# Kernel tuning notes

Measured on AMD Instinct MI355X. Metric: run time of the kernel, lower is better.

The kernel has to match this reference:

```python
import jax, jax.numpy as jnp
import numpy as np

L, D, H, FF = 4, 256, 8, 1024
B, S = 4, 1024
HD = D // H
EPS = 1e-5


def layer_norm(x, g, b):
    mu = jnp.mean(x, axis=-1, keepdims=True)
    var = jnp.mean(jnp.square(x - mu), axis=-1, keepdims=True)
    return (x - mu) * jax.lax.rsqrt(var + EPS) * g + b


def setup_inputs() -> dict:
    key = jax.random.key(0)
    ks = jax.random.split(key, 16)
    sd = 0.02
    return {
        "x": jax.random.normal(ks[0], (B, S, D), dtype=jnp.float32),
        "mask": jnp.ones((B, S), dtype=jnp.int32),
        # per-layer stacked params (leading dim L); Linear stored as (in, out)
        "qkv_w": jax.random.normal(ks[1], (L, D, 3 * D), dtype=jnp.float32) * sd,
        "qkv_b": jnp.zeros((L, 3 * D), dtype=jnp.float32),
        "fc_w": jax.random.normal(ks[2], (L, D, D), dtype=jnp.float32) * sd,
        "fc_b": jnp.zeros((L, D), dtype=jnp.float32),
        "ln1_g": jnp.ones((L, D), dtype=jnp.float32),
        "ln1_b": jnp.zeros((L, D), dtype=jnp.float32),
        "ln2_g": jnp.ones((L, D), dtype=jnp.float32),
        "ln2_b": jnp.zeros((L, D), dtype=jnp.float32),
        "ff1_w": jax.random.normal(ks[3], (L, D, FF), dtype=jnp.float32) * sd,
        "ff1_b": jnp.zeros((L, FF), dtype=jnp.float32),
        "ff2_w": jax.random.normal(ks[4], (L, FF, D), dtype=jnp.float32) * sd,
        "ff2_b": jnp.zeros((L, D), dtype=jnp.float32),
    }


def reference(x, mask, qkv_w, qkv_b, fc_w, fc_b, ln1_g, ln1_b, ln2_g, ln2_b,
              ff1_w, ff1_b, ff2_w, ff2_b):
    # mask: 1 = valid token, 0 = pad
    neg_inf = jnp.finfo(x.dtype).min
    key_mask = (mask == 0)[:, None, None, :]  # [B,1,1,S]
    for l in range(L):
        residual = x
        qkv = x @ qkv_w[l] + qkv_b[l]                       # [B,S,3D]
        q, k, v = jnp.split(qkv, 3, axis=-1)
        q = q.reshape(B, S, H, HD).transpose(0, 2, 1, 3)    # [B,H,S,hd]
        k = k.reshape(B, S, H, HD).transpose(0, 2, 1, 3)
        v = v.reshape(B, S, H, HD).transpose(0, 2, 1, 3)
        attn = jnp.einsum('bhqd,bhkd->bhqk', q, k)          # scale=1 (scale=False)
        attn = jnp.where(key_mask, neg_inf, attn)
        attn = jax.nn.softmax(attn, axis=-1)
        o = jnp.einsum('bhqk,bhkd->bhqd', attn, v)
        o = o.transpose(0, 2, 1, 3).reshape(B, S, D)
        o = o @ fc_w[l] + fc_b[l]
        x = layer_norm(o + residual, ln1_g[l], ln1_b[l])    # after_norm=True
        residual = x
        h = jax.nn.relu(x @ ff1_w[l] + ff1_b[l])
        h = h @ ff2_w[l] + ff2_b[l]
        x = layer_norm(residual + h, ln2_g[l], ln2_b[l])
    return x
```

## Files before the change

kernel.cpp:

```cpp
#include <hip/hip_runtime.h>
#include <hip/hip_bf16.h>
#include <math.h>

#define NL 4
#define DMODEL 256
#define NH 8
#define FFDIM 1024
#define BB 4
#define SS 1024
#define HDIM 32
#define MROWS (BB * SS)
#define LN_EPS 1e-5f

typedef __bf16 bf16x8 __attribute__((ext_vector_type(8)));
typedef float f32x4 __attribute__((ext_vector_type(4)));
typedef short s16x4 __attribute__((ext_vector_type(4)));
typedef unsigned int u32;

__device__ __forceinline__ ushort f2bf(float f) {
    uint u = __builtin_bit_cast(uint, f);
    u += 0x7fff + ((u >> 16) & 1);
    return (ushort)(u >> 16);
}
__device__ __forceinline__ uint pack2(float a, float b) {
    return (uint)f2bf(a) | ((uint)f2bf(b) << 16);
}

__device__ __forceinline__ int xcd_swz(int bid, int nwg) {
    return (bid & 7) * (nwg >> 3) + (bid >> 3);
}

template<int N> __device__ __forceinline__ void vmcnt_wait() {
    asm volatile("s_waitcnt vmcnt(%0)" :: "n"(N) : "memory");
}
__device__ __forceinline__ void raw_barrier() {
    asm volatile("s_barrier" ::: "memory");
}
__device__ __forceinline__ void lgkm0() {
    asm volatile("s_waitcnt lgkmcnt(0)" ::: "memory");
}

__device__ __forceinline__ void async_ld16(const void* g, void* l) {
    __builtin_amdgcn_global_load_lds(
        (const __attribute__((address_space(1))) u32*)g,
        (__attribute__((address_space(3))) u32*)l, 16, 0, 0);
}

#if __has_builtin(__builtin_amdgcn_ds_read_tr16_b64)
#define TR_BUILTIN 1
#else
#define TR_BUILTIN 0
#endif

__device__ __forceinline__ s16x4 tr16(const ushort* p) {
    __attribute__((address_space(3))) s16x4* ap =
        (__attribute__((address_space(3))) s16x4*)p;
#if TR_BUILTIN
    return __builtin_amdgcn_ds_read_tr16_b64(ap);
#else
    s16x4 r;
    asm volatile("ds_read_b64_tr_b16 %0, %1" : "=v"(r) : "v"(ap) : "memory");
    return r;
#endif
}
__device__ __forceinline__ void tr_fence() {
#if !TR_BUILTIN
    asm volatile("s_waitcnt lgkmcnt(0)" ::: "memory");
    __builtin_amdgcn_sched_barrier(0);
#endif
}

__global__ __launch_bounds__(256)
void wconv_all(const float* __restrict__ qkv_w, const float* __restrict__ fc_w,
               const float* __restrict__ ff1_w, const float* __restrict__ ff2_w,
               ushort* __restrict__ wq, ushort* __restrict__ wfc,
               ushort* __restrict__ wf1, ushort* __restrict__ wf2)
{
    const int l = blockIdx.z;
    int t = blockIdx.x;
    const float* src; ushort* dst; int K, N, nx;
    if (t < 192)      {          src = qkv_w; dst = wq;  K = 256;  N = 768;  nx = 24; }
    else if (t < 256) { t -= 192; src = fc_w;  dst = wfc; K = 256;  N = 256;  nx = 8; }
    else if (t < 512) { t -= 256; src = ff1_w; dst = wf1; K = 256;  N = 1024; nx = 32; }
    else              { t -= 512; src = ff2_w; dst = wf2; K = 1024; N = 256;  nx = 8; }
    src += (size_t)l * K * N;
    dst += (size_t)l * K * N;
    const int n0 = (t % nx) * 32, k0 = (t / nx) * 32;

    __shared__ ushort tt[32][33];
    const int tn = threadIdx.x & 31, tk8 = threadIdx.x >> 5;
    #pragma unroll
    for (int i = 0; i < 4; ++i)
        tt[tn][tk8 + i * 8] = f2bf(src[(size_t)(k0 + tk8 + i * 8) * N + n0 + tn]);
    __syncthreads();
    #pragma unroll
    for (int i = 0; i < 4; ++i)
        dst[(size_t)(n0 + tk8 + i * 8) * K + k0 + tn] = tt[tk8 + i * 8][tn];
}

__global__ __launch_bounds__(256)
void convert_x(const float* __restrict__ xin, float* __restrict__ x,
               ushort* __restrict__ xb)
{
    const size_t i = ((size_t)blockIdx.x * 256 + threadIdx.x) * 4;
    const float4 v = *reinterpret_cast<const float4*>(xin + i);
    *reinterpret_cast<float4*>(x + i) = v;
    uint2 p = make_uint2(pack2(v.x, v.y), pack2(v.z, v.w));
    *reinterpret_cast<uint2*>(xb + i) = p;
}

template<int BM, int BN, int WM, int WN, int ACT, int OBF>
__global__ __launch_bounds__(256)
void gemm_mfma(const ushort* __restrict__ A, const ushort* __restrict__ WT,
               const float* __restrict__ bias, float* __restrict__ Cf,
               ushort* __restrict__ Cb, int N, int K)
{
    constexpr int BK = 64;
    constexpr int WR = BM / WM;
    constexpr int WC = BN / WN;
    constexpr int MR = WR / 16, NR = WC / 16;
    constexpr int LSTG = BM / 32 + BN / 32;
    __shared__ __align__(16) ushort As[2][BM * BK];
    __shared__ __align__(16) ushort Bs[2][BN * BK];

    const int tid = threadIdx.x;
    const int lin = blockIdx.y * gridDim.x + blockIdx.x;
    const int work = xcd_swz(lin, gridDim.x * gridDim.y);
    const int m0 = (work / gridDim.x) * BM, n0 = (work % gridDim.x) * BN;
    const int wid = tid >> 6, lane = tid & 63;
    const int g = lane >> 4, c = lane & 15;
    const int wr = wid / WN, wc = wid % WN;

    auto stage = [&](int buf, int k0) {
        #pragma unroll
        for (int it = 0; it < (BM * BK * 2) / 4096; ++it) {
            const int o = tid * 16 + it * 4096;
            const int r = o >> 7;
            const int cb = (o & 127) ^ ((r & 7) << 4);
            async_ld16(A + (size_t)(m0 + r) * K + k0 + (cb >> 1),
                       (char*)&As[buf][0] + o);
        }
        #pragma unroll
        for (int it = 0; it < (BN * BK * 2) / 4096; ++it) {
            const int o = tid * 16 + it * 4096;
            const int r = o >> 7;
            const int cb = (o & 127) ^ ((r & 7) << 4);
            async_ld16(WT + (size_t)(n0 + r) * K + k0 + (cb >> 1),
                       (char*)&Bs[buf][0] + o);
        }
    };

    f32x4 acc[MR][NR] = {};

    stage(0, 0);

    int cur = 0;
    for (int k0 = 0; k0 < K; k0 += BK, cur ^= 1) {
        if (k0 + BK < K) { stage(cur ^ 1, k0 + BK); vmcnt_wait<LSTG>(); }
        else             { vmcnt_wait<0>(); }
        raw_barrier();

        #pragma unroll
        for (int ks = 0; ks < 2; ++ks) {
            bf16x8 af[MR], bfr[NR];
            #pragma unroll
            for (int mi = 0; mi < MR; ++mi) {
                const int row = wr * WR + mi * 16 + c;
                af[mi] = *(const bf16x8*)((const char*)&As[cur][0]
                    + row * 128 + ((ks * 64 + g * 16) ^ ((row & 7) << 4)));
            }
            #pragma unroll
            for (int ni = 0; ni < NR; ++ni) {
                const int row = wc * WC + ni * 16 + c;
                bfr[ni] = *(const bf16x8*)((const char*)&Bs[cur][0]
                    + row * 128 + ((ks * 64 + g * 16) ^ ((row & 7) << 4)));
            }
            #pragma unroll
            for (int mi = 0; mi < MR; ++mi)
                #pragma unroll
                for (int ni = 0; ni < NR; ++ni)
                    acc[mi][ni] = __builtin_amdgcn_mfma_f32_16x16x32_bf16(
                        af[mi], bfr[ni], acc[mi][ni], 0, 0, 0);
        }
        raw_barrier();
    }

    float bv[NR];
    #pragma unroll
    for (int ni = 0; ni < NR; ++ni)
        bv[ni] = bias[n0 + wc * WC + ni * 16 + c];

    #pragma unroll
    for (int mi = 0; mi < MR; ++mi) {
        #pragma unroll
        for (int j = 0; j < 4; ++j) {
            const int row = m0 + wr * WR + mi * 16 + g * 4 + j;
            #pragma unroll
            for (int ni = 0; ni < NR; ++ni) {
                float v = acc[mi][ni][j] + bv[ni];
                if (ACT) v = fmaxf(v, 0.f);
                const int col = n0 + wc * WC + ni * 16 + c;
                if (OBF) Cb[(size_t)row * N + col] = f2bf(v);
                else     Cf[(size_t)row * N + col] = v;
            }
        }
    }
}

__global__ __launch_bounds__(512)
void mlp_fused(const ushort* __restrict__ Aattn, const ushort* __restrict__ Wfc,
               const float* __restrict__ bfc, const float* __restrict__ g1,
               const float* __restrict__ be1, const ushort* __restrict__ W1,
               const float* __restrict__ b1, const ushort* __restrict__ W2,
               const float* __restrict__ b2, const float* __restrict__ g2,
               const float* __restrict__ be2, float* __restrict__ x,
               ushort* __restrict__ xb)
{
    __shared__ __align__(16) ushort As[2][16 * 64];
    __shared__ __align__(16) ushort Bs[2][256 * 64];
    __shared__ __align__(16) ushort ybf[16 * 256];
    __shared__ __align__(16) ushort hbuf[16 * 1024];
    __shared__ float rsum[8][16], rsq[8][16], mval[16], ival[16];

    const int tid = threadIdx.x;
    const int m0 = blockIdx.x * 16;
    const int wid = tid >> 6, lane = tid & 63;
    const int g = lane >> 4, c = lane & 15;

    auto stageB = [&](int buf, const ushort* src, int ldk) {
        #pragma unroll
        for (int it = 0; it < 4; ++it) {
            const int o = tid * 16 + it * 8192;
            const int r = o >> 7;
            const int cb = (o & 127) ^ ((r & 7) << 4);
            async_ld16(src + (size_t)r * ldk + (cb >> 1), (char*)&Bs[buf][0] + o);
        }
    };
    auto stageA = [&](int buf, int k0) {
        if (tid < 128) {
            const int o = tid * 16;
            const int r = o >> 7;
            const int cb = (o & 127) ^ ((r & 7) << 4);
            async_ld16(Aattn + (size_t)(m0 + r) * 256 + k0 + (cb >> 1),
                       (char*)&As[buf][0] + o);
        }
    };

    f32x4 acc[2] = {};

    stageA(0, 0); stageB(0, Wfc, 256);
    int cur = 0;
    #pragma unroll
    for (int k = 0; k < 4; ++k, cur ^= 1) {
        if (k < 3) {
            stageA(cur ^ 1, (k + 1) * 64);
            stageB(cur ^ 1, Wfc + (k + 1) * 64, 256);
            if (tid < 128) vmcnt_wait<5>(); else vmcnt_wait<4>();
        } else {
            stageB(cur ^ 1, W1, 256);
            vmcnt_wait<4>();
        }
        raw_barrier();
        #pragma unroll
        for (int ks = 0; ks < 2; ++ks) {
            const bf16x8 af = *(const bf16x8*)((const char*)&As[cur][0]
                + c * 128 + ((ks * 64 + g * 16) ^ ((c & 7) << 4)));
            #pragma unroll
            for (int ni = 0; ni < 2; ++ni) {
                const int row = wid * 32 + ni * 16 + c;
                const bf16x8 bf = *(const bf16x8*)((const char*)&Bs[cur][0]
                    + row * 128 + ((ks * 64 + g * 16) ^ ((row & 7) << 4)));
                acc[ni] = __builtin_amdgcn_mfma_f32_16x16x32_bf16(af, bf, acc[ni], 0, 0, 0);
            }
        }
        raw_barrier();
    }

    float res[2][4];
    {
        float bv[2], gl[2], bl[2];
        #pragma unroll
        for (int ni = 0; ni < 2; ++ni) {
            const int col = wid * 32 + ni * 16 + c;
            bv[ni] = bfc[col]; gl[ni] = g1[col]; bl[ni] = be1[col];
        }
        #pragma unroll
        for (int j = 0; j < 4; ++j) {
            const int row = g * 4 + j;
            float s = 0.f;
            #pragma unroll
            for (int ni = 0; ni < 2; ++ni) {
                const int col = wid * 32 + ni * 16 + c;
                float vv = acc[ni][j] + bv[ni] + x[(size_t)(m0 + row) * 256 + col];
                acc[ni][j] = vv;
                s += vv;
            }
            #pragma unroll
            for (int off = 1; off < 16; off <<= 1) s += __shfl_xor(s, off);
            if (c == 0) rsum[wid][row] = s;
        }
        __syncthreads();
        if (tid < 16)
            mval[tid] = (rsum[0][tid] + rsum[1][tid] + rsum[2][tid] + rsum[3][tid]
                       + rsum[4][tid] + rsum[5][tid] + rsum[6][tid] + rsum[7][tid])
                        * (1.f / 256);
        __syncthreads();
        #pragma unroll
        for (int j = 0; j < 4; ++j) {
            const int row = g * 4 + j;
            const float mean = mval[row];
            float q = 0.f;
            #pragma unroll
            for (int ni = 0; ni < 2; ++ni) {
                const float d = acc[ni][j] - mean;
                q += d * d;
            }
            #pragma unroll
            for (int off = 1; off < 16; off <<= 1) q += __shfl_xor(q, off);
            if (c == 0) rsq[wid][row] = q;
        }
        __syncthreads();
        if (tid < 16) {
            const float q = rsq[0][tid] + rsq[1][tid] + rsq[2][tid] + rsq[3][tid]
                          + rsq[4][tid] + rsq[5][tid] + rsq[6][tid] + rsq[7][tid];
            ival[tid] = rsqrtf(q * (1.f / 256) + LN_EPS);
        }
        __syncthreads();
        #pragma unroll
        for (int j = 0; j < 4; ++j) {
            const int row = g * 4 + j;
            const float mean = mval[row], inv = ival[row];
            #pragma unroll
            for (int ni = 0; ni < 2; ++ni) {
                const int col = wid * 32 + ni * 16 + c;
                const float y = (acc[ni][j] - mean) * inv * gl[ni] + bl[ni];
                res[ni][j] = y;
                const int byteo = row * 512 + ((col * 2) ^ ((row & 7) << 4));
                *(ushort*)((char*)ybf + byteo) = f2bf(y);
                acc[ni][j] = 0.f;
            }
        }
    }
    lgkm0();
    raw_barrier();

    #pragma unroll 1
    for (int s = 0; s < 16; ++s, cur ^= 1) {
        const int kk = s & 3;
        if (s < 15) {
            const int s2 = s + 1;
            stageB(cur ^ 1, W1 + (size_t)((s2 >> 2) * 256) * 256 + (s2 & 3) * 64, 256);
            vmcnt_wait<4>();
        } else {
            stageB(cur ^ 1, W2, 1024);
            vmcnt_wait<4>();
        }
        raw_barrier();
        #pragma unroll
        for (int ks = 0; ks < 2; ++ks) {
            const int kbyte = (kk * 64 + ks * 32 + g * 8) * 2;
            const bf16x8 af = *(const bf16x8*)((const char*)ybf
                + c * 512 + (kbyte ^ ((c & 7) << 4)));
            #pragma unroll
            for (int ni = 0; ni < 2; ++ni) {
                const int row = wid * 32 + ni * 16 + c;
                const bf16x8 bf = *(const bf16x8*)((const char*)&Bs[cur][0]
                    + row * 128 + ((ks * 64 + g * 16) ^ ((row & 7) << 4)));
                acc[ni] = __builtin_amdgcn_mfma_f32_16x16x32_bf16(af, bf, acc[ni], 0, 0, 0);
            }
        }
        raw_barrier();
        if (kk == 3) {
            const int nt = s >> 2;
            #pragma unroll
            for (int j = 0; j < 4; ++j) {
                const int row = g * 4 + j;
                #pragma unroll
                for (int ni = 0; ni < 2; ++ni) {
                    const int col = nt * 256 + wid * 32 + ni * 16 + c;
                    const float h = fmaxf(acc[ni][j] + b1[col], 0.f);
                    const int byteo = row * 2048 + (((col & 1023) * 2) ^ ((row & 7) << 4));
                    *(ushort*)((char*)hbuf + byteo) = f2bf(h);
                    acc[ni][j] = 0.f;
                }
            }
        }
    }
    lgkm0();
    raw_barrier();

    #pragma unroll 1
    for (int s = 0; s < 16; ++s, cur ^= 1) {
        if (s < 15) { stageB(cur ^ 1, W2 + (s + 1) * 64, 1024); vmcnt_wait<4>(); }
        else        { vmcnt_wait<0>(); }
        raw_barrier();
        #pragma unroll
        for (int ks = 0; ks < 2; ++ks) {
            const int kbyte = (s * 64 + ks * 32 + g * 8) * 2;
            const bf16x8 af = *(const bf16x8*)((const char*)hbuf
                + c * 2048 + (kbyte ^ ((c & 7) << 4)));
            #pragma unroll
            for (int ni = 0; ni < 2; ++ni) {
                const int row = wid * 32 + ni * 16 + c;
                const bf16x8 bf = *(const bf16x8*)((const char*)&Bs[cur][0]
                    + row * 128 + ((ks * 64 + g * 16) ^ ((row & 7) << 4)));
                acc[ni] = __builtin_amdgcn_mfma_f32_16x16x32_bf16(af, bf, acc[ni], 0, 0, 0);
            }
        }
        raw_barrier();
    }

    {
        float bv[2], gl[2], bl[2];
        #pragma unroll
        for (int ni = 0; ni < 2; ++ni) {
            const int col = wid * 32 + ni * 16 + c;
            bv[ni] = b2[col]; gl[ni] = g2[col]; bl[ni] = be2[col];
        }
        #pragma unroll
        for (int j = 0; j < 4; ++j) {
            const int row = g * 4 + j;
            float s = 0.f;
            #pragma unroll
            for (int ni = 0; ni < 2; ++ni) {
                float vv = acc[ni][j] + bv[ni] + res[ni][j];
                acc[ni][j] = vv;
                s += vv;
            }
            #pragma unroll
            for (int off = 1; off < 16; off <<= 1) s += __shfl_xor(s, off);
            if (c == 0) rsum[wid][row] = s;
        }
        __syncthreads();
        if (tid < 16)
            mval[tid] = (rsum[0][tid] + rsum[1][tid] + rsum[2][tid] + rsum[3][tid]
                       + rsum[4][tid] + rsum[5][tid] + rsum[6][tid] + rsum[7][tid])
                        * (1.f / 256);
        __syncthreads();
        #pragma unroll
        for (int j = 0; j < 4; ++j) {
            const int row = g * 4 + j;
            const float mean = mval[row];
            float q = 0.f;
            #pragma unroll
            for (int ni = 0; ni < 2; ++ni) {
                const float d = acc[ni][j] - mean;
                q += d * d;
            }
            #pragma unroll
            for (int off = 1; off < 16; off <<= 1) q += __shfl_xor(q, off);
            if (c == 0) rsq[wid][row] = q;
        }
        __syncthreads();
        if (tid < 16) {
            const float q = rsq[0][tid] + rsq[1][tid] + rsq[2][tid] + rsq[3][tid]
                          + rsq[4][tid] + rsq[5][tid] + rsq[6][tid] + rsq[7][tid];
            ival[tid] = rsqrtf(q * (1.f / 256) + LN_EPS);
        }
        __syncthreads();
        #pragma unroll
        for (int j = 0; j < 4; ++j) {
            const int row = g * 4 + j;
            const float mean = mval[row], inv = ival[row];
            #pragma unroll
            for (int ni = 0; ni < 2; ++ni) {
                const int col = wid * 32 + ni * 16 + c;
                const float y = (acc[ni][j] - mean) * inv * gl[ni] + bl[ni];
                x[(size_t)(m0 + row) * 256 + col] = y;
                xb[(size_t)(m0 + row) * 256 + col] = f2bf(y);
            }
        }
    }
}

__global__ __launch_bounds__(512)
void attn_mfma8(const ushort* __restrict__ qkv, const int* __restrict__ mask,
                ushort* __restrict__ out)
{
    const int tid = threadIdx.x;
    const int lane = tid & 63, wid = tid >> 6;
    const int g = lane >> 4, c = lane & 15;
    const int work = xcd_swz(blockIdx.x, 256);
    const int qblk = work & 7;
    const int bh = work >> 3;
    const int h = bh & (NH - 1), b = bh >> 3;
    const int q0 = qblk * 128 + wid * 16;

    __shared__ __align__(16) ushort Kb[2][128 * 32];
    __shared__ __align__(16) ushort Vs[2][2][128][16];
    __shared__ __align__(16) ushort Pl[8][16][136];
    __shared__ __align__(16) float  sbias[SS];
    __shared__ int mflag[8];

    const ushort* base  = qkv + (size_t)b * SS * 768;
    const ushort* kbase = base + DMODEL + h * HDIM;
    const ushort* vbase = base + 2 * DMODEL + h * HDIM;

    {
        const int i = tid * 2;
        const int2 mv = *reinterpret_cast<const int2*>(mask + b * SS + i);
        float2 bv;
        bv.x = mv.x ? 0.f : -3.4e38f;
        bv.y = mv.y ? 0.f : -3.4e38f;
        *reinterpret_cast<float2*>(&sbias[i]) = bv;
        const int miss = __any(!(mv.x && mv.y));
        if (lane == 0) mflag[wid] = miss;
    }

    const bf16x8 qfrag = *(const bf16x8*)(
        base + (size_t)(q0 + c) * 768 + h * HDIM + g * 8);

    const int o16   = tid * 16;
    const int krow  = o16 >> 6;
    const int kin   = (o16 & 63) ^ ((krow & 3) << 4);
    const int vhalf = o16 >> 12;
    const int vkey  = (o16 & 4095) >> 5;
    const int vd    = vhalf * 16 + (((o16 >> 4) & 1) << 3);

    #define STAGE(buf, koff)                                                   \
        do {                                                                   \
            async_ld16(kbase + (size_t)((koff) + krow) * 768 + (kin >> 1),     \
                       (char*)&Kb[buf][0] + o16);                              \
            async_ld16(vbase + (size_t)((koff) + vkey) * 768 + vd,             \
                       (char*)&Vs[buf][0][0][0] + o16);                        \
        } while (0)

    STAGE(0, 0);
    lgkm0();
    raw_barrier();
    const int anyMasked = mflag[0] | mflag[1] | mflag[2] | mflag[3]
                        | mflag[4] | mflag[5] | mflag[6] | mflag[7];

    float m = -1e30f, lpart = 0.f;
    f32x4 o0 = {0.f, 0.f, 0.f, 0.f}, o1 = {0.f, 0.f, 0.f, 0.f};
    const f32x4 zf = {0.f, 0.f, 0.f, 0.f};

    for (int t = 0; t < 8; ++t) {
        const int cur = t & 1;
        if (t < 7) { STAGE(cur ^ 1, (t + 1) * 128); vmcnt_wait<2>(); }
        else       { vmcnt_wait<0>(); }
        raw_barrier();

        f32x4 s[8];
        __builtin_amdgcn_s_setprio(1);
        #pragma unroll
        for (int kt = 0; kt < 8; ++kt) {
            const int row = kt * 16 + c;
            const bf16x8 kf = *(const bf16x8*)((const char*)&Kb[cur][0]
                + row * 64 + ((g * 16) ^ ((c & 3) << 4)));
            s[kt] = __builtin_amdgcn_mfma_f32_16x16x32_bf16(kf, qfrag, zf, 0, 0, 0);
        }
        __builtin_amdgcn_s_setprio(0);

        if (anyMasked) {
            #pragma unroll
            for (int kt = 0; kt < 8; ++kt) {
                const f32x4 bv = *reinterpret_cast<const f32x4*>(
                    &sbias[t * 128 + kt * 16 + g * 4]);
                #pragma unroll
                for (int r = 0; r < 4; ++r) s[kt][r] += bv[r];
            }
        }

        union UU { s16x4 h[2]; bf16x8 v; };
        UU u0[4], u1[4];
        #pragma unroll
        for (int ks = 0; ks < 4; ++ks) {
            const int vr0 = ks * 32 + g * 8;
            u0[ks].h[0] = tr16(&Vs[cur][0][vr0][c]);
            u0[ks].h[1] = tr16(&Vs[cur][0][vr0 + 4][c]);
            u1[ks].h[0] = tr16(&Vs[cur][1][vr0][c]);
            u1[ks].h[1] = tr16(&Vs[cur][1][vr0 + 4][c]);
        }

        float mx = fmaxf(fmaxf(s[0][0], s[0][1]), fmaxf(s[0][2], s[0][3]));
        #pragma unroll
        for (int kt = 1; kt < 8; ++kt)
            mx = fmaxf(mx, fmaxf(fmaxf(s[kt][0], s[kt][1]),
                                 fmaxf(s[kt][2], s[kt][3])));
        if (!__all(mx <= m + 8.f)) {
            float fm = fmaxf(mx, __shfl_xor(mx, 16));
            fm = fmaxf(fm, __shfl_xor(fm, 32));
            const float mn = fmaxf(m, fm);
            const float sc = __expf(m - mn);
            m = mn;
            lpart *= sc;
            float scr[4];
            #pragma unroll
            for (int r = 0; r < 4; ++r) scr[r] = __shfl(sc, g * 4 + r);
            #pragma unroll
            for (int r = 0; r < 4; ++r) { o0[r] *= scr[r]; o1[r] *= scr[r]; }
        }

        float ls = 0.f;
        #pragma unroll
        for (int kt = 0; kt < 8; ++kt) {
            const float p0 = __expf(s[kt][0] - m);
            const float p1 = __expf(s[kt][1] - m);
            const float p2 = __expf(s[kt][2] - m);
            const float p3 = __expf(s[kt][3] - m);
            ls += (p0 + p1) + (p2 + p3);
            uint2 pk2 = make_uint2(pack2(p0, p1), pack2(p2, p3));
            *reinterpret_cast<uint2*>(&Pl[wid][c][kt * 16 + g * 4]) = pk2;
        }
        lpart += ls;

        tr_fence();
        __builtin_amdgcn_s_setprio(1);
        #pragma unroll
        for (int ks = 0; ks < 4; ++ks) {
            const bf16x8 pa = *(const bf16x8*)&Pl[wid][c][ks * 32 + g * 8];
            o0 = __builtin_amdgcn_mfma_f32_16x16x32_bf16(pa, u0[ks].v, o0, 0, 0, 0);
            o1 = __builtin_amdgcn_mfma_f32_16x16x32_bf16(pa, u1[ks].v, o1, 0, 0, 0);
        }
        __builtin_amdgcn_s_setprio(0);
        raw_barrier();
    }
    #undef STAGE

    float lsum = lpart;
    lsum += __shfl_xor(lsum, 16);
    lsum += __shfl_xor(lsum, 32);
    const float rs = 1.f / lsum;
    float inv[4];
    #pragma unroll
    for (int r = 0; r < 4; ++r) inv[r] = __shfl(rs, g * 4 + r);
    #pragma unroll
    for (int r = 0; r < 4; ++r) {
        ushort* op = out + (size_t)(b * SS + q0 + g * 4 + r) * DMODEL + h * HDIM;
        op[c]      = f2bf(o0[r] * inv[r]);
        op[16 + c] = f2bf(o1[r] * inv[r]);
    }
}

extern "C" void kernel_launch(void* const* d_in, const int* in_sizes, int n_in,
                              void* d_out, int out_size, void* d_ws, size_t ws_size,
                              hipStream_t stream)
{
    const float* x_in   = (const float*)d_in[0];
    const int*   maskp  = (const int*)d_in[1];
    const float* qkv_w  = (const float*)d_in[2];
    const float* qkv_b  = (const float*)d_in[3];
    const float* fc_w   = (const float*)d_in[4];
    const float* fc_b   = (const float*)d_in[5];
    const float* ln1_g  = (const float*)d_in[6];
    const float* ln1_b  = (const float*)d_in[7];
    const float* ln2_g  = (const float*)d_in[8];
    const float* ln2_b  = (const float*)d_in[9];
    const float* ff1_w  = (const float*)d_in[10];
    const float* ff1_b  = (const float*)d_in[11];
    const float* ff2_w  = (const float*)d_in[12];
    const float* ff2_b  = (const float*)d_in[13];

    float* x = (float*)d_out;

    ushort* wt_qkv = (ushort*)d_ws;
    ushort* wt_fc  = wt_qkv + (size_t)NL * 768 * 256;
    ushort* wt_ff1 = wt_fc  + (size_t)NL * 256 * 256;
    ushort* wt_ff2 = wt_ff1 + (size_t)NL * 1024 * 256;
    ushort* big    = wt_ff2 + (size_t)NL * 256 * 1024;
    ushort* attn_bf= big + (size_t)MROWS * FFDIM;
    ushort* x_bf   = attn_bf + (size_t)MROWS * DMODEL;

    wconv_all<<<dim3(768, 1, NL), 256, 0, stream>>>(
        qkv_w, fc_w, ff1_w, ff2_w, wt_qkv, wt_fc, wt_ff1, wt_ff2);
    convert_x<<<dim3(MROWS * DMODEL / 1024), 256, 0, stream>>>(x_in, x, x_bf);

    for (int l = 0; l < NL; ++l) {
        gemm_mfma<64, 64, 2, 2, 0, 1><<<dim3(12, 64), 256, 0, stream>>>(
            x_bf, wt_qkv + (size_t)l * 768 * 256, qkv_b + l * 768,
            nullptr, big, 768, 256);
        attn_mfma8<<<dim3(256), 512, 0, stream>>>(big, maskp, attn_bf);
        mlp_fused<<<dim3(256), 512, 0, stream>>>(
            attn_bf, wt_fc + (size_t)l * 256 * 256, fc_b + l * 256,
            ln1_g + l * DMODEL, ln1_b + l * DMODEL,
            wt_ff1 + (size_t)l * 1024 * 256, ff1_b + l * FFDIM,
            wt_ff2 + (size_t)l * 256 * 1024, ff2_b + l * DMODEL,
            ln2_g + l * DMODEL, ln2_b + l * DMODEL, x, x_bf);
    }
}
```

Measured before the change: 209.2 us.

## Process two query tiles per wave in attention, halving block threads

The attention kernel now uses 4 waves of 256 threads instead of 8 waves, and each wave handles 32 query rows as two 16-row tiles. Each K fragment and each transposed V fragment read from shared memory feeds two MFMAs, which halves LDS reads per unit of work, and each thread issues twice as many async loads per stage. The cost is fewer waves per block for hiding latency and roughly double the register pressure for scores and accumulators, which may lower occupancy.

After: 224.0 us. 7.1% more time.

```diff
diff --git a/kernel.cpp b/kernel.cpp
--- a/kernel.cpp
+++ b/kernel.cpp
@@ -473,8 +473,8 @@
     }
 }
 
-__global__ __launch_bounds__(512)
-void attn_mfma8(const ushort* __restrict__ qkv, const int* __restrict__ mask,
+__global__ __launch_bounds__(256)
+void attn_mfma9(const ushort* __restrict__ qkv, const int* __restrict__ mask,
                 ushort* __restrict__ out)
 {
     const int tid = threadIdx.x;
@@ -484,71 +484,80 @@
     const int qblk = work & 7;
     const int bh = work >> 3;
     const int h = bh & (NH - 1), b = bh >> 3;
-    const int q0 = qblk * 128 + wid * 16;
+    const int q0 = qblk * 128 + wid * 32;
 
     __shared__ __align__(16) ushort Kb[2][128 * 32];
     __shared__ __align__(16) ushort Vs[2][2][128][16];
-    __shared__ __align__(16) ushort Pl[8][16][136];
+    __shared__ __align__(16) ushort Pl[4][2][16][136];
     __shared__ __align__(16) float  sbias[SS];
-    __shared__ int mflag[8];
+    __shared__ int mflag[4];
 
     const ushort* base  = qkv + (size_t)b * SS * 768;
     const ushort* kbase = base + DMODEL + h * HDIM;
     const ushort* vbase = base + 2 * DMODEL + h * HDIM;
 
     {
-        const int i = tid * 2;
-        const int2 mv = *reinterpret_cast<const int2*>(mask + b * SS + i);
-        float2 bv;
+        const int i = tid * 4;
+        const int4 mv = *reinterpret_cast<const int4*>(mask + b * SS + i);
+        float4 bv;
         bv.x = mv.x ? 0.f : -3.4e38f;
         bv.y = mv.y ? 0.f : -3.4e38f;
-        *reinterpret_cast<float2*>(&sbias[i]) = bv;
-        const int miss = __any(!(mv.x && mv.y));
+        bv.z = mv.z ? 0.f : -3.4e38f;
+        bv.w = mv.w ? 0.f : -3.4e38f;
+        *reinterpret_cast<float4*>(&sbias[i]) = bv;
+        const int miss = __any(!(mv.x && mv.y && mv.z && mv.w));
         if (lane == 0) mflag[wid] = miss;
     }
 
-    const bf16x8 qfrag = *(const bf16x8*)(
-        base + (size_t)(q0 + c) * 768 + h * HDIM + g * 8);
-
-    const int o16   = tid * 16;
-    const int krow  = o16 >> 6;
-    const int kin   = (o16 & 63) ^ ((krow & 3) << 4);
-    const int vhalf = o16 >> 12;
-    const int vkey  = (o16 & 4095) >> 5;
-    const int vd    = vhalf * 16 + (((o16 >> 4) & 1) << 3);
-
-    #define STAGE(buf, koff)                                                   \
-        do {                                                                   \
-            async_ld16(kbase + (size_t)((koff) + krow) * 768 + (kin >> 1),     \
-                       (char*)&Kb[buf][0] + o16);                              \
-            async_ld16(vbase + (size_t)((koff) + vkey) * 768 + vd,             \
-                       (char*)&Vs[buf][0][0][0] + o16);                        \
+    bf16x8 qfrag[2];
+    #pragma unroll
+    for (int t = 0; t < 2; ++t)
+        qfrag[t] = *(const bf16x8*)(
+            base + (size_t)(q0 + t * 16 + c) * 768 + h * HDIM + g * 8);
+
+    const int o16 = tid * 16;
+
+    #define STAGE(buf, koff)                                                     \
+        do {                                                                     \
+            _Pragma("unroll")                                                    \
+            for (int it = 0; it < 2; ++it) {                                     \
+                const int off = o16 + it * 4096;                                 \
+                const int krow = off >> 6;                                       \
+                const int kin  = (off & 63) ^ ((krow & 3) << 4);                 \
+                async_ld16(kbase + (size_t)((koff) + krow) * 768 + (kin >> 1),   \
+                           (char*)&Kb[buf][0] + off);                            \
+                const int vhalf = off >> 12;                                     \
+                const int vkey  = (off & 4095) >> 5;                             \
+                const int vd    = vhalf * 16 + (((off >> 4) & 1) << 3);          \
+                async_ld16(vbase + (size_t)((koff) + vkey) * 768 + vd,           \
+                           (char*)&Vs[buf][0][0][0] + off);                      \
+            }                                                                    \
         } while (0)
 
     STAGE(0, 0);
     lgkm0();
     raw_barrier();
-    const int anyMasked = mflag[0] | mflag[1] | mflag[2] | mflag[3]
-                        | mflag[4] | mflag[5] | mflag[6] | mflag[7];
-
-    float m = -1e30f, lpart = 0.f;
-    f32x4 o0 = {0.f, 0.f, 0.f, 0.f}, o1 = {0.f, 0.f, 0.f, 0.f};
+    const int anyMasked = mflag[0] | mflag[1] | mflag[2] | mflag[3];
+
+    float m[2] = { -1e30f, -1e30f }, lpart[2] = { 0.f, 0.f };
+    f32x4 o0[2] = {}, o1[2] = {};
     const f32x4 zf = {0.f, 0.f, 0.f, 0.f};
 
-    for (int t = 0; t < 8; ++t) {
-        const int cur = t & 1;
-        if (t < 7) { STAGE(cur ^ 1, (t + 1) * 128); vmcnt_wait<2>(); }
-        else       { vmcnt_wait<0>(); }
-        raw_barrier();
-
-        f32x4 s[8];
+    for (int tt = 0; tt < 8; ++tt) {
+        const int cur = tt & 1;
+        if (tt < 7) { STAGE(cur ^ 1, (tt + 1) * 128); vmcnt_wait<4>(); }
+        else        { vmcnt_wait<0>(); }
+        raw_barrier();
+
+        f32x4 s[2][8];
         __builtin_amdgcn_s_setprio(1);
         #pragma unroll
         for (int kt = 0; kt < 8; ++kt) {
             const int row = kt * 16 + c;
             const bf16x8 kf = *(const bf16x8*)((const char*)&Kb[cur][0]
                 + row * 64 + ((g * 16) ^ ((c & 3) << 4)));
-            s[kt] = __builtin_amdgcn_mfma_f32_16x16x32_bf16(kf, qfrag, zf, 0, 0, 0);
+            s[0][kt] = __builtin_amdgcn_mfma_f32_16x16x32_bf16(kf, qfrag[0], zf, 0, 0, 0);
+            s[1][kt] = __builtin_amdgcn_mfma_f32_16x16x32_bf16(kf, qfrag[1], zf, 0, 0, 0);
         }
         __builtin_amdgcn_s_setprio(0);
 
@@ -556,9 +565,12 @@
             #pragma unroll
             for (int kt = 0; kt < 8; ++kt) {
                 const f32x4 bv = *reinterpret_cast<const f32x4*>(
-                    &sbias[t * 128 + kt * 16 + g * 4]);
+                    &sbias[tt * 128 + kt * 16 + g * 4]);
                 #pragma unroll
-                for (int r = 0; r < 4; ++r) s[kt][r] += bv[r];
+                for (int r = 0; r < 4; ++r) {
+                    s[0][kt][r] += bv[r];
+                    s[1][kt][r] += bv[r];
+                }
             }
         }
 
@@ -573,63 +585,74 @@
             u1[ks].h[1] = tr16(&Vs[cur][1][vr0 + 4][c]);
         }
 
-        float mx = fmaxf(fmaxf(s[0][0], s[0][1]), fmaxf(s[0][2], s[0][3]));
-        #pragma unroll
-        for (int kt = 1; kt < 8; ++kt)
-            mx = fmaxf(mx, fmaxf(fmaxf(s[kt][0], s[kt][1]),
-                                 fmaxf(s[kt][2], s[kt][3])));
-        if (!__all(mx <= m + 8.f)) {
-            float fm = fmaxf(mx, __shfl_xor(mx, 16));
-            fm = fmaxf(fm, __shfl_xor(fm, 32));
-            const float mn = fmaxf(m, fm);
-            const float sc = __expf(m - mn);
-            m = mn;
-            lpart *= sc;
-            float scr[4];
-            #pragma unroll
-            for (int r = 0; r < 4; ++r) scr[r] = __shfl(sc, g * 4 + r);
-            #pragma unroll
-            for (int r = 0; r < 4; ++r) { o0[r] *= scr[r]; o1[r] *= scr[r]; }
-        }
-
-        float ls = 0.f;
-        #pragma unroll
-        for (int kt = 0; kt < 8; ++kt) {
-            const float p0 = __expf(s[kt][0] - m);
-            const float p1 = __expf(s[kt][1] - m);
-            const float p2 = __expf(s[kt][2] - m);
-            const float p3 = __expf(s[kt][3] - m);
-            ls += (p0 + p1) + (p2 + p3);
-            uint2 pk2 = make_uint2(pack2(p0, p1), pack2(p2, p3));
-            *reinterpret_cast<uint2*>(&Pl[wid][c][kt * 16 + g * 4]) = pk2;
-        }
-        lpart += ls;
+        #pragma unroll
+        for (int t = 0; t < 2; ++t) {
+            float mx = fmaxf(fmaxf(s[t][0][0], s[t][0][1]),
+                             fmaxf(s[t][0][2], s[t][0][3]));
+            #pragma unroll
+            for (int kt = 1; kt < 8; ++kt)
+                mx = fmaxf(mx, fmaxf(fmaxf(s[t][kt][0], s[t][kt][1]),
+                                     fmaxf(s[t][kt][2], s[t][kt][3])));
+            if (!__all(mx <= m[t] + 8.f)) {
+                float fm = fmaxf(mx, __shfl_xor(mx, 16));
+                fm = fmaxf(fm, __shfl_xor(fm, 32));
+                const float mn = fmaxf(m[t], fm);
+                const float sc = __expf(m[t] - mn);
+                m[t] = mn;
+                lpart[t] *= sc;
+                float scr[4];
+                #pragma unroll
+                for (int r = 0; r < 4; ++r) scr[r] = __shfl(sc, g * 4 + r);
+                #pragma unroll
+                for (int r = 0; r < 4; ++r) { o0[t][r] *= scr[r]; o1[t][r] *= scr[r]; }
+            }
+
+            float ls = 0.f;
+            #pragma unroll
+            for (int kt = 0; kt < 8; ++kt) {
+                const float p0 = __expf(s[t][kt][0] - m[t]);
+                const float p1 = __expf(s[t][kt][1] - m[t]);
+                const float p2 = __expf(s[t][kt][2] - m[t]);
+                const float p3 = __expf(s[t][kt][3] - m[t]);
+                ls += (p0 + p1) + (p2 + p3);
+                uint2 pk2 = make_uint2(pack2(p0, p1), pack2(p2, p3));
+                *reinterpret_cast<uint2*>(&Pl[wid][t][c][kt * 16 + g * 4]) = pk2;
+            }
+            lpart[t] += ls;
+        }
 
         tr_fence();
         __builtin_amdgcn_s_setprio(1);
         #pragma unroll
         for (int ks = 0; ks < 4; ++ks) {
-            const bf16x8 pa = *(const bf16x8*)&Pl[wid][c][ks * 32 + g * 8];
-            o0 = __builtin_amdgcn_mfma_f32_16x16x32_bf16(pa, u0[ks].v, o0, 0, 0, 0);
-            o1 = __builtin_amdgcn_mfma_f32_16x16x32_bf16(pa, u1[ks].v, o1, 0, 0, 0);
+            #pragma unroll
+            for (int t = 0; t < 2; ++t) {
+                const bf16x8 pa = *(const bf16x8*)&Pl[wid][t][c][ks * 32 + g * 8];
+                o0[t] = __builtin_amdgcn_mfma_f32_16x16x32_bf16(pa, u0[ks].v, o0[t], 0, 0, 0);
+                o1[t] = __builtin_amdgcn_mfma_f32_16x16x32_bf16(pa, u1[ks].v, o1[t], 0, 0, 0);
+            }
         }
         __builtin_amdgcn_s_setprio(0);
         raw_barrier();
     }
     #undef STAGE
 
-    float lsum = lpart;
-    lsum += __shfl_xor(lsum, 16);
-    lsum += __shfl_xor(lsum, 32);
-    const float rs = 1.f / lsum;
-    float inv[4];
     #pragma unroll
-    for (int r = 0; r < 4; ++r) inv[r] = __shfl(rs, g * 4 + r);
-    #pragma unroll
-    for (int r = 0; r < 4; ++r) {
-        ushort* op = out + (size_t)(b * SS + q0 + g * 4 + r) * DMODEL + h * HDIM;
-        op[c]      = f2bf(o0[r] * inv[r]);
-        op[16 + c] = f2bf(o1[r] * inv[r]);
+    for (int t = 0; t < 2; ++t) {
+        float lsum = lpart[t];
+        lsum += __shfl_xor(lsum, 16);
+        lsum += __shfl_xor(lsum, 32);
+        const float rs = 1.f / lsum;
+        float inv[4];
+        #pragma unroll
+        for (int r = 0; r < 4; ++r) inv[r] = __shfl(rs, g * 4 + r);
+        #pragma unroll
+        for (int r = 0; r < 4; ++r) {
+            ushort* op = out + (size_t)(b * SS + q0 + t * 16 + g * 4 + r) * DMODEL
+                       + h * HDIM;
+            op[c]      = f2bf(o0[t][r] * inv[r]);
+            op[16 + c] = f2bf(o1[t][r] * inv[r]);
+        }
     }
 }
 
@@ -670,7 +693,7 @@
         gemm_mfma<64, 64, 2, 2, 0, 1><<<dim3(12, 64), 256, 0, stream>>>(
             x_bf, wt_qkv + (size_t)l * 768 * 256, qkv_b + l * 768,
             nullptr, big, 768, 256);
-        attn_mfma8<<<dim3(256), 512, 0, stream>>>(big, maskp, attn_bf);
+        attn_mfma9<<<dim3(256), 256, 0, stream>>>(big, maskp, attn_bf);
         mlp_fused<<<dim3(256), 512, 0, stream>>>(
             attn_bf, wt_fc + (size_t)l * 256 * 256, fc_b + l * 256,
             ln1_g + l * DMODEL, ln1_b + l * DMODEL,
```
